# Performance work log

Measured on AMD Instinct MI355X. Metric: run time of the kernel, lower is better.

The kernel has to match this reference:

```python
import jax, jax.numpy as jnp
import numpy as np

V = 49688; D = 128; Hd = 256; DM = 2 * Hd; FF = 4 * Hd; NH = 4
B = 256; O = 32; L = 32

def _ln(x, g, b, eps=1e-5):
    m = x.mean(-1, keepdims=True)
    v = x.var(-1, keepdims=True)
    return (x - m) / jnp.sqrt(v + eps) * g + b

def _mha(x, in_w, in_b, out_w, out_b, nh):
    Bx, S, E = x.shape
    hd = E // nh
    qkv = x @ in_w.T + in_b
    q, k, v = jnp.split(qkv, 3, axis=-1)
    sp = lambda t: t.reshape(Bx, S, nh, hd).transpose(0, 2, 1, 3)
    q, k, v = sp(q), sp(k), sp(v)
    s = jnp.einsum('bhqd,bhkd->bhqk', q, k) / jnp.sqrt(jnp.asarray(hd, x.dtype))
    o = jnp.einsum('bhqk,bhkd->bhqd', jax.nn.softmax(s, -1), v)
    o = o.transpose(0, 2, 1, 3).reshape(Bx, S, E)
    return o @ out_w.T + out_b

def _gru_dir(x, wih, whh, bih, bhh):
    Bx, T, _ = x.shape
    H = whh.shape[1]
    def step(h, xt):
        gi = xt @ wih.T + bih
        gh = h @ whh.T + bhh
        ir, iz, inn = jnp.split(gi, 3, -1)
        hr, hz, hn = jnp.split(gh, 3, -1)
        r = jax.nn.sigmoid(ir + hr)
        z = jax.nn.sigmoid(iz + hz)
        n = jnp.tanh(inn + r * hn)
        h = (1 - z) * n + z * h
        return h, h
    _, hs = jax.lax.scan(step, jnp.zeros((Bx, H), x.dtype), jnp.swapaxes(x, 0, 1))
    return jnp.swapaxes(hs, 0, 1)

def setup_inputs():
    key = jax.random.key(0)
    it = iter(jax.random.split(key, 48))
    def nrm(shape, s=0.05):
        return jax.random.normal(next(it), shape, jnp.float32) * s
    inp = {}
    inp['order_history'] = jax.random.randint(next(it), (B, O, L), 0, V + 1)
    inp['days_between'] = jax.random.uniform(next(it), (B, O - 1), jnp.float32) * 30.0
    inp['days_since_last'] = jax.random.uniform(next(it), (B,), jnp.float32) * 30.0
    inp['emb'] = nrm((V + 1, D), 1.0).at[0].set(0.0)  # padding_idx=0 -> zero row
    inp['a_in_w'] = nrm((3 * D, D)); inp['a_in_b'] = jnp.zeros((3 * D,))
    inp['a_out_w'] = nrm((D, D)); inp['a_out_b'] = jnp.zeros((D,))
    for d in ('f', 'b'):
        inp['g_wih_' + d] = nrm((3 * Hd, D)); inp['g_whh_' + d] = nrm((3 * Hd, Hd))
        inp['g_bih_' + d] = jnp.zeros((3 * Hd,)); inp['g_bhh_' + d] = jnp.zeros((3 * Hd,))
    inp['t_in_w'] = nrm((3 * DM, DM)); inp['t_in_b'] = jnp.zeros((3 * DM,))
    inp['t_out_w'] = nrm((DM, DM)); inp['t_out_b'] = jnp.zeros((DM,))
    inp['t_ln1_g'] = jnp.ones((DM,)); inp['t_ln1_b'] = jnp.zeros((DM,))
    inp['t_ff1_w'] = nrm((FF, DM)); inp['t_ff1_b'] = jnp.zeros((FF,))
    inp['t_ff2_w'] = nrm((DM, FF)); inp['t_ff2_b'] = jnp.zeros((DM,))
    inp['t_ln2_g'] = jnp.ones((DM,)); inp['t_ln2_b'] = jnp.zeros((DM,))
    inp['te1_w'] = nrm((Hd // 4, 2)); inp['te1_b'] = jnp.zeros((Hd // 4,))
    inp['te_ln1_g'] = jnp.ones((Hd // 4,)); inp['te_ln1_b'] = jnp.zeros((Hd // 4,))
    inp['te2_w'] = nrm((Hd // 2, Hd // 4)); inp['te2_b'] = jnp.zeros((Hd // 2,))
    inp['te_ln2_g'] = jnp.ones((Hd // 2,)); inp['te_ln2_b'] = jnp.zeros((Hd // 2,))
    inp['c_w'] = nrm((Hd, 2 * Hd + Hd // 2)); inp['c_b'] = jnp.zeros((Hd,))
    inp['c_ln_g'] = jnp.ones((Hd,)); inp['c_ln_b'] = jnp.zeros((Hd,))
    return inp

def reference(order_history, days_between, days_since_last, emb, a_in_w, a_in_b, a_out_w, a_out_b, g_wih_f, g_whh_f, g_bih_f, g_bhh_f, g_wih_b, g_whh_b, g_bih_b, g_bhh_b, t_in_w, t_in_b, t_out_w, t_out_b, t_ln1_g, t_ln1_b, t_ff1_w, t_ff1_b, t_ff2_w, t_ff2_b, t_ln2_g, t_ln2_b, te1_w, te1_b, te_ln1_g, te_ln1_b, te2_w, te2_b, te_ln2_g, te_ln2_b, c_w, c_b, c_ln_g, c_ln_b):
    Bx, Ox, Lx = order_history.shape
    # per-order item self-attention, batched over all (user, order) pairs
    x = emb[order_history].reshape(Bx * Ox, Lx, -1)                  # [B*O, L, D]
    x = _mha(x, a_in_w, a_in_b, a_out_w, a_out_b, NH)
    order_emb = x.mean(1).reshape(Bx, Ox, -1)                        # [B, O, D]
    # bidirectional GRU over the order sequence
    hf = _gru_dir(order_emb, g_wih_f, g_whh_f, g_bih_f, g_bhh_f)
    hb = _gru_dir(order_emb[:, ::-1], g_wih_b, g_whh_b, g_bih_b, g_bhh_b)[:, ::-1]
    g = jnp.concatenate([hf, hb], -1)                                # [B, O, 2H]
    # post-LN TransformerEncoderLayer (relu, dropout in eval mode)
    a = _mha(g, t_in_w, t_in_b, t_out_w, t_out_b, NH)
    g = _ln(g + a, t_ln1_g, t_ln1_b)
    f = jax.nn.relu(g @ t_ff1_w.T + t_ff1_b) @ t_ff2_w.T + t_ff2_b
    g = _ln(g + f, t_ln2_g, t_ln2_b)
    enc = g.mean(1)                                                  # [B, 2H]
    # temporal features: only days_mean and recency are used (std computed but unused in original)
    feats = jnp.stack([days_between.mean(1), days_since_last], 1)    # [B, 2]
    te = jax.nn.relu(_ln(feats @ te1_w.T + te1_b, te_ln1_g, te_ln1_b))
    te = jax.nn.relu(_ln(te @ te2_w.T + te2_b, te_ln2_g, te_ln2_b))  # [B, H/2]
    out = jax.nn.relu(_ln(jnp.concatenate([enc, te], 1) @ c_w.T + c_b, c_ln_g, c_ln_b))
    return out                                                       # [B, H]
```

## Files before the change

kernel.cpp:

```cpp
#include <hip/hip_runtime.h>
#include <hip/hip_bf16.h>
#include <math.h>

typedef __hip_bfloat16 bf16;
typedef __attribute__((ext_vector_type(8))) short short8v;
typedef __attribute__((ext_vector_type(4))) short short4v;
typedef __attribute__((ext_vector_type(4))) float float4v;
#define MFMA16 __builtin_amdgcn_mfma_f32_16x16x32_bf16

__device__ __forceinline__ float us2f(unsigned short u) {
  union { unsigned u; float f; } c; c.u = ((unsigned)u) << 16; return c.f;
}
__device__ __forceinline__ unsigned short f2us(float f) {
  return __bfloat16_as_ushort(__float2bfloat16(f));
}

__device__ __forceinline__ float dot_ff(const float* __restrict__ x,
                                        const float* __restrict__ w, int K) {
  const float4* xp = reinterpret_cast<const float4*>(x);
  const float4* wp = reinterpret_cast<const float4*>(w);
  float acc = 0.f;
  const int n = K >> 2;
  for (int i = 0; i < n; ++i) {
    float4 a = xp[i], b = wp[i];
    acc += a.x*b.x + a.y*b.y + a.z*b.z + a.w*b.w;
  }
  return acc;
}

__device__ __forceinline__ float sigm(float x) { return 1.f / (1.f + __expf(-x)); }
__device__ __forceinline__ float tanh_fast(float x) {
  x = fminf(fmaxf(x, -15.f), 15.f);
  float e = __expf(2.f * x);
  return (e - 1.f) / (e + 1.f);
}

__global__ void k_canary(float* __restrict__ out) {
  out[blockIdx.x * 256 + threadIdx.x] = 100.0f;
}

__global__ __launch_bounds__(256) void k_cvt(
    const float* __restrict__ a_in_w, const float* __restrict__ t_in_w,
    const float* __restrict__ t_out_w, const float* __restrict__ t_ff1w,
    const float* __restrict__ t_ff2w, const float* __restrict__ a_out_w,
    unsigned short* __restrict__ awb, unsigned short* __restrict__ twb,
    unsigned short* __restrict__ pwb, unsigned short* __restrict__ f1wb,
    unsigned short* __restrict__ f2wb, unsigned short* __restrict__ awb2)
{
  int i = blockIdx.x * 256 + threadIdx.x;
  if (i < 49152)  awb[i] = f2us(a_in_w[i]);
  if (i < 786432) twb[i] = f2us(t_in_w[i]);
  if (i < 262144) pwb[i] = f2us(t_out_w[i]);
  if (i < 524288) f1wb[i] = f2us(t_ff1w[i]);
  if (i < 524288) f2wb[i] = f2us(t_ff2w[i]);
  if (i < 16384)  awb2[i] = f2us(a_out_w[i]);
}

__global__ __launch_bounds__(256) void k_gru_wb(
    const float* __restrict__ wih_f, const float* __restrict__ whh_f,
    const float* __restrict__ wih_b, const float* __restrict__ whh_b,
    unsigned short* __restrict__ whhb, unsigned short* __restrict__ wihb)
{
  int i = blockIdx.x * 256 + threadIdx.x;
  if (i >= 393216) return;
  int dir = i / 196608, r = i % 196608;
  whhb[i] = f2us((dir ? whh_b : whh_f)[r]);
  if (r < 98304) wihb[dir * 98304 + r] = f2us((dir ? wih_b : wih_f)[r]);
}

__global__ __launch_bounds__(256, 2) void k_qkvpre(
    const float* __restrict__ emb, const unsigned short* __restrict__ awb,
    const float* __restrict__ in_b,
    unsigned short* __restrict__ qkt, unsigned short* __restrict__ vt)
{
  const int row0 = blockIdx.x * 32, tid = threadIdx.x;
  __shared__ alignas(16) unsigned short xs[32 * 136];
  for (int i = tid; i < 1024; i += 256) {
    int t = i >> 5, c4 = (i & 31) << 2;
    int grow = row0 + t; if (grow > 49688) grow = 49688;
    float4 e4 = *reinterpret_cast<const float4*>(emb + (size_t)grow * 128 + c4);
    short4v s; s[0] = f2us(e4.x); s[1] = f2us(e4.y); s[2] = f2us(e4.z); s[3] = f2us(e4.w);
    *reinterpret_cast<short4v*>(xs + t * 136 + c4) = s;
  }
  __syncthreads();
  const int lane = tid & 63, wave = tid >> 6;
  const int l15 = lane & 15, quad = lane >> 4;
  short8v af[2][4];
#pragma unroll
  for (int mt = 0; mt < 2; ++mt)
#pragma unroll
    for (int kc = 0; kc < 4; ++kc)
      af[mt][kc] = *reinterpret_cast<const short8v*>(
          xs + (mt * 16 + l15) * 136 + kc * 32 + quad * 8);
  for (int ni = 0; ni < 6; ++ni) {
    const int j = (wave + ni * 4) * 16 + l15;
    const unsigned short* wrow = awb + (size_t)j * 128;
    float4v acc0 = {0.f, 0.f, 0.f, 0.f}, acc1 = {0.f, 0.f, 0.f, 0.f};
#pragma unroll
    for (int kc = 0; kc < 4; ++kc) {
      short8v bfr = *reinterpret_cast<const short8v*>(wrow + kc * 32 + quad * 8);
      acc0 = MFMA16(af[0][kc], bfr, acc0, 0, 0, 0);
      acc1 = MFMA16(af[1][kc], bfr, acc1, 0, 0, 0);
    }
    const float bj = in_b[j];
#pragma unroll
    for (int r = 0; r < 4; ++r) {
      int g0 = row0 + quad * 4 + r, g1 = g0 + 16;
      if (j < 256) {
        if (g0 <= 49688) qkt[(size_t)g0 * 256 + j] = f2us(acc0[r] + bj);
        if (g1 <= 49688) qkt[(size_t)g1 * 256 + j] = f2us(acc1[r] + bj);
      } else {
        int jj = j - 256;
        if (g0 <= 49688) vt[(size_t)g0 * 128 + jj] = f2us(acc0[r] + bj);
        if (g1 <= 49688) vt[(size_t)g1 * 128 + jj] = f2us(acc1[r] + bj);
      }
    }
  }
}

__global__ __launch_bounds__(256, 5) void k_order_attn(
    const int* __restrict__ oh, const unsigned short* __restrict__ qkt,
    const unsigned short* __restrict__ vt,
    const unsigned short* __restrict__ awb2, const float* __restrict__ out_b,
    unsigned short* __restrict__ oeb)
{
  const int bo = blockIdx.x;
  const int tid = threadIdx.x;
  __shared__ alignas(16) unsigned short qb[32 * 136];
  __shared__ alignas(16) unsigned short kb[32 * 136];
  __shared__ alignas(16) unsigned short vTb[128 * 32];
  unsigned short* ob = qb;
  unsigned short* pb = kb;

  const int lane = tid & 63, wave = tid >> 6;
  const int l15 = lane & 15, quad = lane >> 4;

  for (int i = tid; i < 1024; i += 256) {
    int t = i >> 5, c8 = (i & 31) << 3;
    int id = oh[bo * 32 + t];
    short8v v8 = *reinterpret_cast<const short8v*>(qkt + (size_t)id * 256 + c8);
    if (c8 < 128) *reinterpret_cast<short8v*>(qb + t * 136 + c8) = v8;
    else          *reinterpret_cast<short8v*>(kb + t * 136 + (c8 - 128)) = v8;
  }
  for (int i = tid; i < 512; i += 256) {
    int t = i >> 4, c8 = (i & 15) << 3;
    int id = oh[bo * 32 + t];
    short8v v8 = *reinterpret_cast<const short8v*>(vt + (size_t)id * 128 + c8);
#pragma unroll
    for (int j2 = 0; j2 < 8; ++j2) vTb[(c8 + j2) * 32 + t] = v8[j2];
  }
  __syncthreads();
  {
    const int h = wave;
    const float scale1 = 0.17677669529663687f;
    short8v qf[2], kf[2];
#pragma unroll
    for (int mt = 0; mt < 2; ++mt)
      qf[mt] = *reinterpret_cast<const short8v*>(qb + (mt * 16 + l15) * 136 + h * 32 + quad * 8);
#pragma unroll
    for (int nt = 0; nt < 2; ++nt)
      kf[nt] = *reinterpret_cast<const short8v*>(kb + (nt * 16 + l15) * 136 + h * 32 + quad * 8);
    float4v sacc[2][2];
#pragma unroll
    for (int mt = 0; mt < 2; ++mt)
#pragma unroll
      for (int nt = 0; nt < 2; ++nt) {
        sacc[mt][nt] = (float4v){0.f, 0.f, 0.f, 0.f};
        sacc[mt][nt] = MFMA16(qf[mt], kf[nt], sacc[mt][nt], 0, 0, 0);
      }
    __syncthreads();
#pragma unroll
    for (int mt = 0; mt < 2; ++mt)
#pragma unroll
      for (int r = 0; r < 4; ++r) {
        float e0 = __expf(sacc[mt][0][r] * scale1);
        float e1 = __expf(sacc[mt][1][r] * scale1);
        int row = h * 32 + mt * 16 + quad * 4 + r;
        pb[row * 32 + l15] = f2us(e0);
        pb[row * 32 + 16 + l15] = f2us(e1);
      }
    short8v ones;
#pragma unroll
    for (int i = 0; i < 8; ++i) ones[i] = (short)0x3F80;
    short8v pf[2], vf[2];
#pragma unroll
    for (int mt = 0; mt < 2; ++mt)
      pf[mt] = *reinterpret_cast<const short8v*>(pb + (h * 32 + mt * 16 + l15) * 32 + quad * 8);
    float4v sums[2];
#pragma unroll
    for (int mt = 0; mt < 2; ++mt) {
      sums[mt] = (float4v){0.f, 0.f, 0.f, 0.f};
      sums[mt] = MFMA16(pf[mt], ones, sums[mt], 0, 0, 0);
    }
#pragma unroll
    for (int nt = 0; nt < 2; ++nt)
      vf[nt] = *reinterpret_cast<const short8v*>(vTb + (h * 32 + nt * 16 + l15) * 32 + quad * 8);
    float4v oacc[2][2];
#pragma unroll
    for (int mt = 0; mt < 2; ++mt)
#pragma unroll
      for (int nt = 0; nt < 2; ++nt) {
        oacc[mt][nt] = (float4v){0.f, 0.f, 0.f, 0.f};
        oacc[mt][nt] = MFMA16(pf[mt], vf[nt], oacc[mt][nt], 0, 0, 0);
      }
#pragma unroll
    for (int mt = 0; mt < 2; ++mt)
#pragma unroll
      for (int r = 0; r < 4; ++r) {
        int t = mt * 16 + quad * 4 + r;
        float inv = 1.f / sums[mt][r];
#pragma unroll
        for (int nt = 0; nt < 2; ++nt)
          ob[t * 136 + h * 32 + nt * 16 + l15] = f2us(oacc[mt][nt][r] * inv);
      }
  }
  __syncthreads();
  {
    float4v acc[2][2];
#pragma unroll
    for (int mt = 0; mt < 2; ++mt)
#pragma unroll
      for (int nt = 0; nt < 2; ++nt) acc[mt][nt] = (float4v){0.f, 0.f, 0.f, 0.f};
#pragma unroll
    for (int kc = 0; kc < 4; ++kc) {
      short8v af0 = *reinterpret_cast<const short8v*>(ob + l15 * 136 + kc * 32 + quad * 8);
      short8v af1 = *reinterpret_cast<const short8v*>(ob + (16 + l15) * 136 + kc * 32 + quad * 8);
#pragma unroll
      for (int nt = 0; nt < 2; ++nt) {
        int j = (wave * 2 + nt) * 16 + l15;
        short8v bfr = *reinterpret_cast<const short8v*>(awb2 + (size_t)j * 128 + kc * 32 + quad * 8);
        acc[0][nt] = MFMA16(af0, bfr, acc[0][nt], 0, 0, 0);
        acc[1][nt] = MFMA16(af1, bfr, acc[1][nt], 0, 0, 0);
      }
    }
#pragma unroll
    for (int nt = 0; nt < 2; ++nt) {
      float part = 0.f;
#pragma unroll
      for (int mt = 0; mt < 2; ++mt)
#pragma unroll
        for (int r = 0; r < 4; ++r) part += acc[mt][nt][r];
      part += __shfl_xor(part, 16);
      part += __shfl_xor(part, 32);
      if (quad == 0) {
        int j = (wave * 2 + nt) * 16 + l15;
        oeb[(size_t)bo * 128 + j] = f2us(part * (1.f / 32.f) + out_b[j]);
      }
    }
  }
}

__global__ __launch_bounds__(256, 2) void k_gru_gi(
    const unsigned short* __restrict__ oeb, const unsigned short* __restrict__ wihb,
    unsigned short* __restrict__ gi)
{
  const int row0 = blockIdx.x * 32, tid = threadIdx.x;
  __shared__ alignas(16) unsigned short xs[32 * 136];
  for (int i = tid; i < 512; i += 256) {
    int t = i >> 4, c8 = (i & 15) << 3;
    *reinterpret_cast<short8v*>(xs + t * 136 + c8) =
        *reinterpret_cast<const short8v*>(oeb + (size_t)(row0 + t) * 128 + c8);
  }
  __syncthreads();
  const int lane = tid & 63, wave = tid >> 6;
  const int l15 = lane & 15, quad = lane >> 4;
  short8v af[2][4];
#pragma unroll
  for (int mt = 0; mt < 2; ++mt)
#pragma unroll
    for (int kc = 0; kc < 4; ++kc)
      af[mt][kc] = *reinterpret_cast<const short8v*>(
          xs + (mt * 16 + l15) * 136 + kc * 32 + quad * 8);
  for (int ni = 0; ni < 24; ++ni) {
    int col = (wave + ni * 4) * 16 + l15;
    const unsigned short* wrow = wihb + (size_t)col * 128;
    float4v a0 = {0.f,0.f,0.f,0.f}, a1 = {0.f,0.f,0.f,0.f};
#pragma unroll
    for (int kc = 0; kc < 4; ++kc) {
      short8v bfr = *reinterpret_cast<const short8v*>(wrow + kc * 32 + quad * 8);
      a0 = MFMA16(af[0][kc], bfr, a0, 0, 0, 0);
      a1 = MFMA16(af[1][kc], bfr, a1, 0, 0, 0);
    }
#pragma unroll
    for (int r = 0; r < 4; ++r) {
      gi[(size_t)(row0 + quad * 4 + r) * 1536 + col] = f2us(a0[r]);
      gi[(size_t)(row0 + quad * 4 + r + 16) * 1536 + col] = f2us(a1[r]);
    }
  }
}

__global__ __launch_bounds__(512, 2) void k_gru_rec(
    const unsigned short* __restrict__ gi, const unsigned short* __restrict__ whhb,
    const float* __restrict__ bih_f, const float* __restrict__ bhh_f,
    const float* __restrict__ bih_b, const float* __restrict__ bhh_b,
    float* __restrict__ g)
{
  const int b0 = blockIdx.x * 2, dir = blockIdx.y;
  const int tid = threadIdx.x;
  const unsigned short* wb = whhb + (size_t)dir * 196608;
  const float* bih = dir ? bih_b : bih_f;
  const float* bhh = dir ? bhh_b : bhh_f;
  __shared__ alignas(16) unsigned short hb[16 * 264];
  __shared__ float pg[2 * 772];
  const int lane = tid & 63, wave = tid >> 6;
  const int l15 = lane & 15, quad = lane >> 4;
  const int j = tid & 255, mb = tid >> 8;
  const float bir = bih[j], biz = bih[256 + j], bin_ = bih[512 + j];
  const float bhr = bhh[j], bhz = bhh[256 + j], bhn  = bhh[512 + j];
  short8v wf[6][8];
  int cols[6];
#pragma unroll
  for (int ni = 0; ni < 6; ++ni) {
    cols[ni] = (wave + ni * 8) * 16 + l15;
#pragma unroll
    for (int kc = 0; kc < 8; ++kc)
      wf[ni][kc] = *reinterpret_cast<const short8v*>(
          wb + (size_t)cols[ni] * 256 + kc * 32 + quad * 8);
  }
  for (int i = tid; i < 16 * 264; i += 512) hb[i] = 0;
  int tcur = dir ? 31 : 0;
  size_t gbase = ((size_t)(b0 + mb) * 32 + tcur) * 1536 + dir * 768;
  float gr = us2f(gi[gbase + j]);
  float gz = us2f(gi[gbase + 256 + j]);
  float gn = us2f(gi[gbase + 512 + j]);
  __syncthreads();
  for (int s = 0; s < 32; ++s) {
    float4v acc[6];
#pragma unroll
    for (int ni = 0; ni < 6; ++ni) acc[ni] = (float4v){0.f, 0.f, 0.f, 0.f};
#pragma unroll
    for (int kc = 0; kc < 8; ++kc) {
      short8v af = *reinterpret_cast<const short8v*>(hb + l15 * 264 + kc * 32 + quad * 8);
#pragma unroll
      for (int ni = 0; ni < 6; ++ni)
        acc[ni] = MFMA16(af, wf[ni][kc], acc[ni], 0, 0, 0);
    }
    if (quad == 0) {
#pragma unroll
      for (int ni = 0; ni < 6; ++ni) {
        pg[cols[ni]] = acc[ni][0];
        pg[772 + cols[ni]] = acc[ni][1];
      }
    }
    float gr2 = 0.f, gz2 = 0.f, gn2 = 0.f;
    if (s < 31) {
      int t2 = dir ? (30 - s) : (s + 1);
      size_t gb2 = ((size_t)(b0 + mb) * 32 + t2) * 1536 + dir * 768;
      gr2 = us2f(gi[gb2 + j]);
      gz2 = us2f(gi[gb2 + 256 + j]);
      gn2 = us2f(gi[gb2 + 512 + j]);
    }
    __syncthreads();
    {
      const int tt = dir ? (31 - s) : s;
      float hprev = us2f(hb[mb * 264 + j]);
      float r = sigm(gr + bir + pg[mb * 772 + j] + bhr);
      float z = sigm(gz + biz + pg[mb * 772 + 256 + j] + bhz);
      float n = tanh_fast(gn + bin_ + r * (pg[mb * 772 + 512 + j] + bhn));
      float nh = (1.f - z) * n + z * hprev;
      hb[mb * 264 + j] = f2us(nh);
      g[((size_t)(b0 + mb) * 32 + tt) * 512 + dir * 256 + j] = nh;
    }
    gr = gr2; gz = gz2; gn = gn2;
    __syncthreads();
  }
}

__global__ __launch_bounds__(256, 4) void k_mha2f(
    const float* __restrict__ g, const unsigned short* __restrict__ twb,
    const float* __restrict__ Bv, float* __restrict__ attn)
{
  const int b = blockIdx.x, h = blockIdx.y, tid = threadIdx.x;
  __shared__ alignas(16) unsigned short xs3[32 * 136];
  __shared__ alignas(16) unsigned short qk[2 * 32 * 136];
  __shared__ alignas(16) unsigned short vT[128 * 40];
  unsigned short* qs = qk;
  unsigned short* ks = qk + 32 * 136;
  unsigned short* pb = xs3;
  const int lane = tid & 63, wave = tid >> 6;
  const int l15 = lane & 15, quad = lane >> 4;

  int wrowi[6];
#pragma unroll
  for (int ni = 0; ni < 6; ++ni) {
    int idx = (wave + ni * 4) * 16 + l15;
    int m = idx >> 7, dd = idx & 127;
    wrowi[ni] = m * 512 + h * 128 + dd;
  }
  float4v acc[6][2];
#pragma unroll
  for (int ni = 0; ni < 6; ++ni)
#pragma unroll
    for (int mt = 0; mt < 2; ++mt) acc[ni][mt] = (float4v){0.f, 0.f, 0.f, 0.f};

  for (int ck = 0; ck < 4; ++ck) {
    __syncthreads();
    for (int i = tid; i < 1024; i += 256) {
      int t = i >> 5, c4 = (i & 31) << 2;
      float4 e4 = *reinterpret_cast<const float4*>(
          g + (size_t)b * 16384 + t * 512 + ck * 128 + c4);
      short4v s; s[0] = f2us(e4.x); s[1] = f2us(e4.y); s[2] = f2us(e4.z); s[3] = f2us(e4.w);
      *reinterpret_cast<short4v*>(xs3 + t * 136 + c4) = s;
    }
    __syncthreads();
    short8v af2[2][4];
#pragma unroll
    for (int mt = 0; mt < 2; ++mt)
#pragma unroll
      for (int u = 0; u < 4; ++u)
        af2[mt][u] = *reinterpret_cast<const short8v*>(
            xs3 + (mt * 16 + l15) * 136 + u * 32 + quad * 8);
#pragma unroll
    for (int ni = 0; ni < 6; ++ni) {
      const unsigned short* wrow = twb + (size_t)wrowi[ni] * 512 + ck * 128;
#pragma unroll
      for (int u = 0; u < 4; ++u) {
        short8v bfr = *reinterpret_cast<const short8v*>(wrow + u * 32 + quad * 8);
        acc[ni][0] = MFMA16(af2[0][u], bfr, acc[ni][0], 0, 0, 0);
        acc[ni][1] = MFMA16(af2[1][u], bfr, acc[ni][1], 0, 0, 0);
      }
    }
  }
  __syncthreads();
#pragma unroll
  for (int ni = 0; ni < 6; ++ni) {
    int idx = (wave + ni * 4) * 16 + l15;
    int m = idx >> 7, dd = idx & 127;
    float bj = Bv[wrowi[ni]];
    if (m < 2) {
      unsigned short* dst = (m == 0) ? qs : ks;
#pragma unroll
      for (int r = 0; r < 4; ++r) {
        int t0 = quad * 4 + r;
        dst[t0 * 136 + dd] = f2us(acc[ni][0][r] + bj);
        dst[(t0 + 16) * 136 + dd] = f2us(acc[ni][1][r] + bj);
      }
    } else {
      short4v s0, s1;
#pragma unroll
      for (int r = 0; r < 4; ++r) { s0[r] = f2us(acc[ni][0][r] + bj); s1[r] = f2us(acc[ni][1][r] + bj); }
      *reinterpret_cast<short4v*>(vT + dd * 40 + quad * 4) = s0;
      *reinterpret_cast<short4v*>(vT + dd * 40 + 16 + quad * 4) = s1;
    }
  }
  __syncthreads();
  {
    const float scale2 = 0.08838834764831845f;
    const int mt = wave >> 1, nt = wave & 1;
    float4v a = {0.f, 0.f, 0.f, 0.f};
#pragma unroll
    for (int kc = 0; kc < 4; ++kc) {
      short8v qf = *reinterpret_cast<const short8v*>(qs + (mt * 16 + l15) * 136 + kc * 32 + quad * 8);
      short8v kf = *reinterpret_cast<const short8v*>(ks + (nt * 16 + l15) * 136 + kc * 32 + quad * 8);
      a = MFMA16(qf, kf, a, 0, 0, 0);
    }
#pragma unroll
    for (int r = 0; r < 4; ++r) {
      int row = mt * 16 + quad * 4 + r;
      pb[row * 32 + nt * 16 + l15] = f2us(__expf(a[r] * scale2));
    }
  }
  __syncthreads();
  {
    short8v ones;
#pragma unroll
    for (int i = 0; i < 8; ++i) ones[i] = (short)0x3F80;
    short8v pf[2], vf[2];
#pragma unroll
    for (int mt = 0; mt < 2; ++mt)
      pf[mt] = *reinterpret_cast<const short8v*>(pb + (mt * 16 + l15) * 32 + quad * 8);
    float4v sums[2];
#pragma unroll
    for (int mt = 0; mt < 2; ++mt) {
      sums[mt] = (float4v){0.f, 0.f, 0.f, 0.f};
      sums[mt] = MFMA16(pf[mt], ones, sums[mt], 0, 0, 0);
    }
#pragma unroll
    for (int ntl = 0; ntl < 2; ++ntl)
      vf[ntl] = *reinterpret_cast<const short8v*>(vT + ((2 * wave + ntl) * 16 + l15) * 40 + quad * 8);
    float4v oacc[2][2];
#pragma unroll
    for (int mt = 0; mt < 2; ++mt)
#pragma unroll
      for (int ntl = 0; ntl < 2; ++ntl) {
        oacc[mt][ntl] = (float4v){0.f, 0.f, 0.f, 0.f};
        oacc[mt][ntl] = MFMA16(pf[mt], vf[ntl], oacc[mt][ntl], 0, 0, 0);
      }
#pragma unroll
    for (int mt = 0; mt < 2; ++mt)
#pragma unroll
      for (int r = 0; r < 4; ++r) {
        int q = mt * 16 + quad * 4 + r;
        float inv = 1.f / sums[mt][r];
#pragma unroll
        for (int ntl = 0; ntl < 2; ++ntl)
          attn[((size_t)b * 32 + q) * 512 + h * 128 + (2 * wave + ntl) * 16 + l15] =
              oacc[mt][ntl][r] * inv;
      }
  }
}

__global__ __launch_bounds__(512, 2) void k_projln_mfma(
    const float* __restrict__ X, const unsigned short* __restrict__ Wb,
    const float* __restrict__ bias, const float* __restrict__ res,
    const float* __restrict__ gam, const float* __restrict__ bet,
    float* __restrict__ Y)
{
  const int row0 = blockIdx.x * 16, tid = threadIdx.x;
  __shared__ alignas(16) unsigned short xs[16 * 520];
  __shared__ float ys[16 * 516];
  for (int i = tid; i < 16 * 512; i += 512) {
    int t = i >> 9, c = i & 511;
    xs[t * 520 + c] = f2us(X[(size_t)(row0 + t) * 512 + c]);
  }
  __syncthreads();
  {
    const int lane = tid & 63, wave = tid >> 6;
    const int l15 = lane & 15, quad = lane >> 4;
    short8v af[16];
#pragma unroll
    for (int kc = 0; kc < 16; ++kc)
      af[kc] = *reinterpret_cast<const short8v*>(xs + l15 * 520 + kc * 32 + quad * 8);
    for (int ni = 0; ni < 4; ++ni) {
      int col = (wave + ni * 8) * 16 + l15;
      const unsigned short* wrow = Wb + (size_t)col * 512;
      float4v acc = {0.f,0.f,0.f,0.f};
#pragma unroll
      for (int kc = 0; kc < 16; ++kc) {
        short8v bfr = *reinterpret_cast<const short8v*>(wrow + kc * 32 + quad * 8);
        acc = MFMA16(af[kc], bfr, acc, 0, 0, 0);
      }
      float bj = bias[col];
#pragma unroll
      for (int r = 0; r < 4; ++r)
        ys[(quad * 4 + r) * 516 + col] = acc[r] + bj;
    }
  }
  __syncthreads();
  for (int i = tid; i < 16 * 512; i += 512) {
    int t = i >> 9, c = i & 511;
    ys[t * 516 + c] += res[(size_t)(row0 + t) * 512 + c];
  }
  __syncthreads();
  {
    int row = tid >> 5, l32 = tid & 31;
    const float* yr = ys + row * 516;
    float part = 0.f;
#pragma unroll
    for (int k = 0; k < 16; ++k) part += yr[l32 + 32 * k];
#pragma unroll
    for (int off = 16; off; off >>= 1) part += __shfl_xor(part, off, 32);
    float mean = part * (1.f / 512.f);
    float var = 0.f;
#pragma unroll
    for (int k = 0; k < 16; ++k) { float d = yr[l32 + 32 * k] - mean; var += d * d; }
#pragma unroll
    for (int off = 16; off; off >>= 1) var += __shfl_xor(var, off, 32);
    float rs = rsqrtf(var * (1.f / 512.f) + 1e-5f);
    for (int k = 0; k < 16; ++k) {
      int c = l32 + 32 * k;
      Y[(size_t)(row0 + row) * 512 + c] = (yr[c] - mean) * rs * gam[c] + bet[c];
    }
  }
}

__global__ __launch_bounds__(512, 2) void k_ffln(
    const float* __restrict__ X, const unsigned short* __restrict__ W1,
    const float* __restrict__ b1, const unsigned short* __restrict__ W2,
    const float* __restrict__ b2, const float* __restrict__ res,
    const float* __restrict__ gam, const float* __restrict__ bet,
    float* __restrict__ Y)
{
  const int row0 = blockIdx.x * 16, tid = threadIdx.x;
  __shared__ alignas(16) unsigned short xs[16 * 520];
  __shared__ alignas(16) unsigned short f1L[16 * 1032];
  float* ys = reinterpret_cast<float*>(f1L);
  const int lane = tid & 63, wave = tid >> 6;
  const int l15 = lane & 15, quad = lane >> 4;
  for (int i = tid; i < 16 * 512; i += 512) {
    int t = i >> 9, c = i & 511;
    xs[t * 520 + c] = f2us(X[(size_t)(row0 + t) * 512 + c]);
  }
  __syncthreads();
  for (int ni = 0; ni < 8; ++ni) {
    int col = (wave + ni * 8) * 16 + l15;
    const unsigned short* wrow = W1 + (size_t)col * 512;
    float4v acc = {0.f,0.f,0.f,0.f};
#pragma unroll
    for (int kc = 0; kc < 16; ++kc) {
      short8v a = *reinterpret_cast<const short8v*>(xs + l15 * 520 + kc * 32 + quad * 8);
      short8v bfr = *reinterpret_cast<const short8v*>(wrow + kc * 32 + quad * 8);
      acc = MFMA16(a, bfr, acc, 0, 0, 0);
    }
    float bj = b1[col];
#pragma unroll
    for (int r = 0; r < 4; ++r)
      f1L[(quad * 4 + r) * 1032 + col] = f2us(fmaxf(acc[r] + bj, 0.f));
  }
  __syncthreads();
  float4v acc2[4];
#pragma unroll
  for (int ni = 0; ni < 4; ++ni) acc2[ni] = (float4v){0.f,0.f,0.f,0.f};
  int cols2[4];
#pragma unroll
  for (int ni = 0; ni < 4; ++ni) cols2[ni] = (wave + ni * 8) * 16 + l15;
  for (int half = 0; half < 2; ++half) {
    for (int kc = 0; kc < 16; ++kc) {
      short8v a = *reinterpret_cast<const short8v*>(
          f1L + l15 * 1032 + half * 512 + kc * 32 + quad * 8);
#pragma unroll
      for (int ni = 0; ni < 4; ++ni) {
        short8v bfr = *reinterpret_cast<const short8v*>(
            W2 + (size_t)cols2[ni] * 1024 + half * 512 + kc * 32 + quad * 8);
        acc2[ni] = MFMA16(a, bfr, acc2[ni], 0, 0, 0);
      }
    }
  }
  __syncthreads();
  for (int ni = 0; ni < 4; ++ni) {
    int col = cols2[ni];
    float bj = b2[col];
#pragma unroll
    for (int r = 0; r < 4; ++r)
      ys[(quad * 4 + r) * 516 + col] = acc2[ni][r] + bj;
  }
  __syncthreads();
  for (int i = tid; i < 16 * 512; i += 512) {
    int t = i >> 9, c = i & 511;
    ys[t * 516 + c] += res[(size_t)(row0 + t) * 512 + c];
  }
  __syncthreads();
  {
    int row = tid >> 5, l32 = tid & 31;
    const float* yr = ys + row * 516;
    float part = 0.f;
#pragma unroll
    for (int k = 0; k < 16; ++k) part += yr[l32 + 32 * k];
#pragma unroll
    for (int off = 16; off; off >>= 1) part += __shfl_xor(part, off, 32);
    float mean = part * (1.f / 512.f);
    float var = 0.f;
#pragma unroll
    for (int k = 0; k < 16; ++k) { float d = yr[l32 + 32 * k] - mean; var += d * d; }
#pragma unroll
    for (int off = 16; off; off >>= 1) var += __shfl_xor(var, off, 32);
    float rs = rsqrtf(var * (1.f / 512.f) + 1e-5f);
    for (int k = 0; k < 16; ++k) {
      int c = l32 + 32 * k;
      Y[(size_t)(row0 + row) * 512 + c] = (yr[c] - mean) * rs * gam[c] + bet[c];
    }
  }
}

__global__ __launch_bounds__(256) void k_final(
    const float* __restrict__ g2,
    const float* __restrict__ db, const float* __restrict__ dsl,
    const float* __restrict__ te1_w, const float* __restrict__ te1_b,
    const float* __restrict__ l1g, const float* __restrict__ l1b,
    const float* __restrict__ te2_w, const float* __restrict__ te2_b,
    const float* __restrict__ l2g, const float* __restrict__ l2b,
    const float* __restrict__ c_w, const float* __restrict__ c_b,
    const float* __restrict__ clg, const float* __restrict__ clb,
    float* __restrict__ out)
{
  const int b = blockIdx.x, tid = threadIdx.x;
  __shared__ float cat[640];
  __shared__ float t1[64];
  __shared__ float t2[128];
  __shared__ float pre[256];
  __shared__ float red[256];
  __shared__ float st[2];
  for (int i = tid; i < 512; i += 256) {
    float acc = 0.f;
#pragma unroll
    for (int t = 0; t < 32; ++t) acc += g2[((size_t)b * 32 + t) * 512 + i];
    cat[i] = acc * (1.f / 32.f);
  }
  if (tid == 0) {
    float s = 0.f;
    for (int i = 0; i < 31; ++i) s += db[b * 31 + i];
    st[0] = s / 31.f;
    st[1] = dsl[b];
  }
  __syncthreads();
  const float f0 = st[0], f1v = st[1];
  if (tid < 64)
    t1[tid] = f0 * te1_w[tid * 2] + f1v * te1_w[tid * 2 + 1] + te1_b[tid];
  __syncthreads();
  if (tid == 0) {
    float m = 0.f; for (int i = 0; i < 64; ++i) m += t1[i]; m *= (1.f / 64.f);
    float v = 0.f; for (int i = 0; i < 64; ++i) { float d = t1[i] - m; v += d * d; }
    st[0] = m; st[1] = rsqrtf(v * (1.f / 64.f) + 1e-5f);
  }
  __syncthreads();
  if (tid < 64) {
    float v = (t1[tid] - st[0]) * st[1] * l1g[tid] + l1b[tid];
    t1[tid] = fmaxf(v, 0.f);
  }
  __syncthreads();
  if (tid < 128)
    t2[tid] = dot_ff(t1, te2_w + (size_t)tid * 64, 64) + te2_b[tid];
  __syncthreads();
  if (tid == 0) {
    float m = 0.f; for (int i = 0; i < 128; ++i) m += t2[i]; m *= (1.f / 128.f);
    float v = 0.f; for (int i = 0; i < 128; ++i) { float d = t2[i] - m; v += d * d; }
    st[0] = m; st[1] = rsqrtf(v * (1.f / 128.f) + 1e-5f);
  }
  __syncthreads();
  if (tid < 128) {
    float v = (t2[tid] - st[0]) * st[1] * l2g[tid] + l2b[tid];
    cat[512 + tid] = fmaxf(v, 0.f);
  }
  __syncthreads();
  pre[tid] = dot_ff(cat, c_w + (size_t)tid * 640, 640) + c_b[tid];
  red[tid] = pre[tid];
  __syncthreads();
  for (int s = 128; s > 0; s >>= 1) { if (tid < s) red[tid] += red[tid + s]; __syncthreads(); }
  const float m = red[0] * (1.f / 256.f);
  __syncthreads();
  const float d = pre[tid] - m;
  red[tid] = d * d;
  __syncthreads();
  for (int s = 128; s > 0; s >>= 1) { if (tid < s) red[tid] += red[tid + s]; __syncthreads(); }
  const float rs = rsqrtf(red[0] * (1.f / 256.f) + 1e-5f);
  float v = d * rs * clg[tid] + clb[tid];
  out[(size_t)b * 256 + tid] = fmaxf(v, 0.f);
}

extern "C" void kernel_launch(void* const* d_in, const int* in_sizes, int n_in,
                              void* d_out, int out_size, void* d_ws, size_t ws_size,
                              hipStream_t stream) {
  (void)in_sizes; (void)n_in; (void)out_size; (void)ws_size;
  const int*   oh     = (const int*)  d_in[0];
  const float* db     = (const float*)d_in[1];
  const float* dsl    = (const float*)d_in[2];
  const float* emb    = (const float*)d_in[3];
  const float* a_in_w = (const float*)d_in[4];
  const float* a_in_b = (const float*)d_in[5];
  const float* a_out_w= (const float*)d_in[6];
  const float* a_out_b= (const float*)d_in[7];
  const float* wih_f  = (const float*)d_in[8];
  const float* whh_f  = (const float*)d_in[9];
  const float* bih_f  = (const float*)d_in[10];
  const float* bhh_f  = (const float*)d_in[11];
  const float* wih_b  = (const float*)d_in[12];
  const float* whh_b  = (const float*)d_in[13];
  const float* bih_b  = (const float*)d_in[14];
  const float* bhh_b  = (const float*)d_in[15];
  const float* t_in_w = (const float*)d_in[16];
  const float* t_in_b = (const float*)d_in[17];
  const float* t_out_w= (const float*)d_in[18];
  const float* t_out_b= (const float*)d_in[19];
  const float* t_ln1g = (const float*)d_in[20];
  const float* t_ln1b = (const float*)d_in[21];
  const float* t_ff1w = (const float*)d_in[22];
  const float* t_ff1b = (const float*)d_in[23];
  const float* t_ff2w = (const float*)d_in[24];
  const float* t_ff2b = (const float*)d_in[25];
  const float* t_ln2g = (const float*)d_in[26];
  const float* t_ln2b = (const float*)d_in[27];
  const float* te1_w  = (const float*)d_in[28];
  const float* te1_b  = (const float*)d_in[29];
  const float* tl1g   = (const float*)d_in[30];
  const float* tl1b   = (const float*)d_in[31];
  const float* te2_w  = (const float*)d_in[32];
  const float* te2_b  = (const float*)d_in[33];
  const float* tl2g   = (const float*)d_in[34];
  const float* tl2b   = (const float*)d_in[35];
  const float* c_w    = (const float*)d_in[36];
  const float* c_b    = (const float*)d_in[37];
  const float* clng   = (const float*)d_in[38];
  const float* clnb   = (const float*)d_in[39];

  float* ws = (float*)d_ws;
  unsigned short* oeb  = (unsigned short*)ws;
  unsigned short* qkt  = (unsigned short*)(ws + 1048576);
  float* g    = ws + 1048576;
  float* attn = ws + 5242880;
  float* g1   = attn;
  float* g2   = attn;
  unsigned short* whhb = (unsigned short*)(ws + 9437184);
  unsigned short* wihb = (unsigned short*)(ws + 9633792);
  unsigned short* awb2 = (unsigned short*)(ws + 9732096);
  unsigned short* awb  = (unsigned short*)(ws + 10027008);
  unsigned short* twb  = (unsigned short*)(ws + 10051584);
  unsigned short* pwb  = (unsigned short*)(ws + 10444800);
  unsigned short* f1wb = (unsigned short*)(ws + 10575872);
  unsigned short* f2wb = (unsigned short*)(ws + 10838016);
  unsigned short* vt   = (unsigned short*)(ws + 11100160);
  unsigned short* gi   = (unsigned short*)(ws + 11100160);

  k_canary<<<256, 256, 0, stream>>>((float*)d_out);
  k_cvt<<<3072, 256, 0, stream>>>(a_in_w, t_in_w, t_out_w, t_ff1w, t_ff2w, a_out_w,
                                  awb, twb, pwb, f1wb, f2wb, awb2);
  k_gru_wb<<<1536, 256, 0, stream>>>(wih_f, whh_f, wih_b, whh_b, whhb, wihb);
  k_qkvpre<<<1553, 256, 0, stream>>>(emb, awb, a_in_b, qkt, vt);
  k_order_attn<<<8192, 256, 0, stream>>>(oh, qkt, vt, awb2, a_out_b, oeb);
  k_gru_gi<<<256, 256, 0, stream>>>(oeb, wihb, gi);
  k_gru_rec<<<dim3(128, 2), 512, 0, stream>>>(gi, whhb, bih_f, bhh_f, bih_b, bhh_b, g);
  k_mha2f<<<dim3(256, 4), 256, 0, stream>>>(g, twb, t_in_b, attn);
  k_projln_mfma<<<512, 512, 0, stream>>>(attn, pwb, t_out_b, g, t_ln1g, t_ln1b, g1);
  k_ffln<<<512, 512, 0, stream>>>(g1, f1wb, t_ff1b, f2wb, t_ff2b, g1,
                                  t_ln2g, t_ln2b, g2);
  k_final<<<256, 256, 0, stream>>>(g2, db, dsl, te1_w, te1_b, tl1g, tl1b,
                                   te2_w, te2_b, tl2g, tl2b, c_w, c_b, clng, clnb,
                                   (float*)d_out);
}
```

Before: 575.1 us.

## Split FF into 32-row chunked GEMM kernel plus separate residual-LayerNorm kernel

The fused FF+LN kernel becomes two kernels. The FF kernel processes 32 rows per block, so each weight load feeds two MFMA tiles. It interleaves FF1 and FF2 over 128-column chunks of the hidden layer, which keeps shared memory small, and it writes raw FF2 output to workspace. A new kernel applies the residual add and LayerNorm. The projection+LN kernel also double-buffers weight-row loads across its column iterations to overlap global loads with MFMA. In exchange this adds an extra global round trip for the FF output, one more launch, and more sync points per chunk.

```diff
diff --git a/kernel.cpp b/kernel.cpp
--- a/kernel.cpp
+++ b/kernel.cpp
@@ -521,15 +521,28 @@
 #pragma unroll
     for (int kc = 0; kc < 16; ++kc)
       af[kc] = *reinterpret_cast<const short8v*>(xs + l15 * 520 + kc * 32 + quad * 8);
+    short8v bufA[16], bufB[16];
+    {
+      const unsigned short* w0 = Wb + (size_t)((wave + 0 * 8) * 16 + l15) * 512;
+#pragma unroll
+      for (int kc = 0; kc < 16; ++kc)
+        bufA[kc] = *reinterpret_cast<const short8v*>(w0 + kc * 32 + quad * 8);
+    }
+#pragma unroll
     for (int ni = 0; ni < 4; ++ni) {
+      short8v* cur = (ni & 1) ? bufB : bufA;
+      short8v* nxt = (ni & 1) ? bufA : bufB;
+      if (ni < 3) {
+        const unsigned short* wn = Wb + (size_t)((wave + (ni + 1) * 8) * 16 + l15) * 512;
+#pragma unroll
+        for (int kc = 0; kc < 16; ++kc)
+          nxt[kc] = *reinterpret_cast<const short8v*>(wn + kc * 32 + quad * 8);
+      }
+      float4v acc = {0.f,0.f,0.f,0.f};
+#pragma unroll
+      for (int kc = 0; kc < 16; ++kc)
+        acc = MFMA16(af[kc], cur[kc], acc, 0, 0, 0);
       int col = (wave + ni * 8) * 16 + l15;
-      const unsigned short* wrow = Wb + (size_t)col * 512;
-      float4v acc = {0.f,0.f,0.f,0.f};
-#pragma unroll
-      for (int kc = 0; kc < 16; ++kc) {
-        short8v bfr = *reinterpret_cast<const short8v*>(wrow + kc * 32 + quad * 8);
-        acc = MFMA16(af[kc], bfr, acc, 0, 0, 0);
-      }
       float bj = bias[col];
 #pragma unroll
       for (int r = 0; r < 4; ++r)
@@ -564,89 +577,110 @@
   }
 }
 
-__global__ __launch_bounds__(512, 2) void k_ffln(
+__global__ __launch_bounds__(512, 2) void k_ff(
     const float* __restrict__ X, const unsigned short* __restrict__ W1,
     const float* __restrict__ b1, const unsigned short* __restrict__ W2,
-    const float* __restrict__ b2, const float* __restrict__ res,
+    const float* __restrict__ b2, float* __restrict__ yraw)
+{
+  const int row0 = blockIdx.x * 32, tid = threadIdx.x;
+  __shared__ alignas(16) unsigned short xs[32 * 520];
+  __shared__ alignas(16) unsigned short f1c[32 * 136];
+  const int lane = tid & 63, wave = tid >> 6;
+  const int l15 = lane & 15, quad = lane >> 4;
+  for (int i = tid; i < 4096; i += 512) {
+    int t = i >> 7, c4 = (i & 127) << 2;
+    float4 e4 = *reinterpret_cast<const float4*>(X + (size_t)(row0 + t) * 512 + c4);
+    short4v s; s[0] = f2us(e4.x); s[1] = f2us(e4.y); s[2] = f2us(e4.z); s[3] = f2us(e4.w);
+    *reinterpret_cast<short4v*>(xs + t * 520 + c4) = s;
+  }
+  __syncthreads();
+  float4v acc2[2][4];
+#pragma unroll
+  for (int mt = 0; mt < 2; ++mt)
+#pragma unroll
+    for (int ni = 0; ni < 4; ++ni) acc2[mt][ni] = (float4v){0.f,0.f,0.f,0.f};
+  int cols2[4];
+#pragma unroll
+  for (int ni = 0; ni < 4; ++ni) cols2[ni] = (wave + ni * 8) * 16 + l15;
+
+  for (int ck = 0; ck < 8; ++ck) {
+    {
+      const int col = ck * 128 + wave * 16 + l15;
+      const unsigned short* wrow = W1 + (size_t)col * 512;
+      float4v a0 = {0.f,0.f,0.f,0.f}, a1 = {0.f,0.f,0.f,0.f};
+#pragma unroll
+      for (int kc = 0; kc < 16; ++kc) {
+        short8v b = *reinterpret_cast<const short8v*>(wrow + kc * 32 + quad * 8);
+        short8v x0 = *reinterpret_cast<const short8v*>(xs + l15 * 520 + kc * 32 + quad * 8);
+        short8v x1 = *reinterpret_cast<const short8v*>(xs + (16 + l15) * 520 + kc * 32 + quad * 8);
+        a0 = MFMA16(x0, b, a0, 0, 0, 0);
+        a1 = MFMA16(x1, b, a1, 0, 0, 0);
+      }
+      const float bj = b1[col];
+      const int cl = wave * 16 + l15;
+#pragma unroll
+      for (int r = 0; r < 4; ++r) {
+        f1c[(quad * 4 + r) * 136 + cl] = f2us(fmaxf(a0[r] + bj, 0.f));
+        f1c[(16 + quad * 4 + r) * 136 + cl] = f2us(fmaxf(a1[r] + bj, 0.f));
+      }
+    }
+    __syncthreads();
+#pragma unroll
+    for (int ni = 0; ni < 4; ++ni) {
+      const unsigned short* wrow2 = W2 + (size_t)cols2[ni] * 1024 + ck * 128;
+#pragma unroll
+      for (int kc = 0; kc < 4; ++kc) {
+        short8v b = *reinterpret_cast<const short8v*>(wrow2 + kc * 32 + quad * 8);
+        short8v a0 = *reinterpret_cast<const short8v*>(f1c + l15 * 136 + kc * 32 + quad * 8);
+        short8v a1 = *reinterpret_cast<const short8v*>(f1c + (16 + l15) * 136 + kc * 32 + quad * 8);
+        acc2[0][ni] = MFMA16(a0, b, acc2[0][ni], 0, 0, 0);
+        acc2[1][ni] = MFMA16(a1, b, acc2[1][ni], 0, 0, 0);
+      }
+    }
+    __syncthreads();
+  }
+#pragma unroll
+  for (int mt = 0; mt < 2; ++mt)
+#pragma unroll
+    for (int ni = 0; ni < 4; ++ni) {
+      int col = cols2[ni];
+      float bj = b2[col];
+#pragma unroll
+      for (int r = 0; r < 4; ++r)
+        yraw[(size_t)(row0 + mt * 16 + quad * 4 + r) * 512 + col] = acc2[mt][ni][r] + bj;
+    }
+}
+
+__global__ __launch_bounds__(256, 2) void k_resln(
+    const float* __restrict__ yraw, const float* __restrict__ res,
     const float* __restrict__ gam, const float* __restrict__ bet,
     float* __restrict__ Y)
 {
   const int row0 = blockIdx.x * 16, tid = threadIdx.x;
-  __shared__ alignas(16) unsigned short xs[16 * 520];
-  __shared__ alignas(16) unsigned short f1L[16 * 1032];
-  float* ys = reinterpret_cast<float*>(f1L);
-  const int lane = tid & 63, wave = tid >> 6;
-  const int l15 = lane & 15, quad = lane >> 4;
-  for (int i = tid; i < 16 * 512; i += 512) {
+  __shared__ float ys[16 * 516];
+  for (int i = tid; i < 16 * 512; i += 256) {
     int t = i >> 9, c = i & 511;
-    xs[t * 520 + c] = f2us(X[(size_t)(row0 + t) * 512 + c]);
-  }
-  __syncthreads();
-  for (int ni = 0; ni < 8; ++ni) {
-    int col = (wave + ni * 8) * 16 + l15;
-    const unsigned short* wrow = W1 + (size_t)col * 512;
-    float4v acc = {0.f,0.f,0.f,0.f};
-#pragma unroll
-    for (int kc = 0; kc < 16; ++kc) {
-      short8v a = *reinterpret_cast<const short8v*>(xs + l15 * 520 + kc * 32 + quad * 8);
-      short8v bfr = *reinterpret_cast<const short8v*>(wrow + kc * 32 + quad * 8);
-      acc = MFMA16(a, bfr, acc, 0, 0, 0);
-    }
-    float bj = b1[col];
-#pragma unroll
-    for (int r = 0; r < 4; ++r)
-      f1L[(quad * 4 + r) * 1032 + col] = f2us(fmaxf(acc[r] + bj, 0.f));
-  }
-  __syncthreads();
-  float4v acc2[4];
-#pragma unroll
-  for (int ni = 0; ni < 4; ++ni) acc2[ni] = (float4v){0.f,0.f,0.f,0.f};
-  int cols2[4];
-#pragma unroll
-  for (int ni = 0; ni < 4; ++ni) cols2[ni] = (wave + ni * 8) * 16 + l15;
-  for (int half = 0; half < 2; ++half) {
-    for (int kc = 0; kc < 16; ++kc) {
-      short8v a = *reinterpret_cast<const short8v*>(
-          f1L + l15 * 1032 + half * 512 + kc * 32 + quad * 8);
-#pragma unroll
-      for (int ni = 0; ni < 4; ++ni) {
-        short8v bfr = *reinterpret_cast<const short8v*>(
-            W2 + (size_t)cols2[ni] * 1024 + half * 512 + kc * 32 + quad * 8);
-        acc2[ni] = MFMA16(a, bfr, acc2[ni], 0, 0, 0);
-      }
-    }
-  }
-  __syncthreads();
-  for (int ni = 0; ni < 4; ++ni) {
-    int col = cols2[ni];
-    float bj = b2[col];
-#pragma unroll
-    for (int r = 0; r < 4; ++r)
-      ys[(quad * 4 + r) * 516 + col] = acc2[ni][r] + bj;
-  }
-  __syncthreads();
-  for (int i = tid; i < 16 * 512; i += 512) {
-    int t = i >> 9, c = i & 511;
-    ys[t * 516 + c] += res[(size_t)(row0 + t) * 512 + c];
+    ys[t * 516 + c] = yraw[(size_t)(row0 + t) * 512 + c] +
+                      res[(size_t)(row0 + t) * 512 + c];
   }
   __syncthreads();
   {
-    int row = tid >> 5, l32 = tid & 31;
+    int row = tid >> 4, l16 = tid & 15;
     const float* yr = ys + row * 516;
     float part = 0.f;
 #pragma unroll
-    for (int k = 0; k < 16; ++k) part += yr[l32 + 32 * k];
-#pragma unroll
-    for (int off = 16; off; off >>= 1) part += __shfl_xor(part, off, 32);
+    for (int k = 0; k < 32; ++k) part += yr[l16 + 16 * k];
+#pragma unroll
+    for (int off = 8; off; off >>= 1) part += __shfl_xor(part, off, 16);
     float mean = part * (1.f / 512.f);
     float var = 0.f;
 #pragma unroll
-    for (int k = 0; k < 16; ++k) { float d = yr[l32 + 32 * k] - mean; var += d * d; }
-#pragma unroll
-    for (int off = 16; off; off >>= 1) var += __shfl_xor(var, off, 32);
+    for (int k = 0; k < 32; ++k) { float d = yr[l16 + 16 * k] - mean; var += d * d; }
+#pragma unroll
+    for (int off = 8; off; off >>= 1) var += __shfl_xor(var, off, 16);
     float rs = rsqrtf(var * (1.f / 512.f) + 1e-5f);
-    for (int k = 0; k < 16; ++k) {
-      int c = l32 + 32 * k;
+    for (int k = 0; k < 32; ++k) {
+      int c = l16 + 16 * k;
       Y[(size_t)(row0 + row) * 512 + c] = (yr[c] - mean) * rs * gam[c] + bet[c];
     }
   }
@@ -776,6 +810,7 @@
   unsigned short* oeb  = (unsigned short*)ws;
   unsigned short* qkt  = (unsigned short*)(ws + 1048576);
   float* g    = ws + 1048576;
+  float* yraw = ws + 1048576;
   float* attn = ws + 5242880;
   float* g1   = attn;
   float* g2   = attn;
@@ -800,8 +835,8 @@
   k_gru_rec<<<dim3(128, 2), 512, 0, stream>>>(gi, whhb, bih_f, bhh_f, bih_b, bhh_b, g);
   k_mha2f<<<dim3(256, 4), 256, 0, stream>>>(g, twb, t_in_b, attn);
   k_projln_mfma<<<512, 512, 0, stream>>>(attn, pwb, t_out_b, g, t_ln1g, t_ln1b, g1);
-  k_ffln<<<512, 512, 0, stream>>>(g1, f1wb, t_ff1b, f2wb, t_ff2b, g1,
-                                  t_ln2g, t_ln2b, g2);
+  k_ff<<<256, 512, 0, stream>>>(g1, f1wb, t_ff1b, f2wb, t_ff2b, yraw);
+  k_resln<<<512, 256, 0, stream>>>(yraw, g1, t_ln2g, t_ln2b, g2);
   k_final<<<256, 256, 0, stream>>>(g2, db, dsl, te1_w, te1_b, tl1g, tl1b,
                                    te2_w, te2_b, tl2g, tl2b, c_w, c_b, clng, clnb,
                                    (float*)d_out);
```

Measured after the change: 547.7 us. -4.8%, faster.
